# Kernel optimization log

Hardware: AMD Instinct MI355X
Metric: run time of the kernel (lower is better)

Reference implementation:

```python
import jax, jax.numpy as jnp
import numpy as np

N = 50000
E = 800000
D_IN = 64
D_E = 32
H = 128
EPS = 1e-5


def _seg_mean(msgs, dst, n):
    s = jax.ops.segment_sum(msgs, dst, num_segments=n)
    c = jax.ops.segment_sum(jnp.ones((dst.shape[0], 1), msgs.dtype), dst, num_segments=n)
    return s / jnp.maximum(c, 1.0)


def _bn(h, g, b, m, v):
    return g * (h - m) * jax.lax.rsqrt(v + EPS) + b


def setup_inputs() -> dict:
    key = jax.random.key(0)
    ks = jax.random.split(key, 32)
    inp = {
        "x": jax.random.normal(ks[0], (N, D_IN), jnp.float32),
        "edge_index_0": jax.random.randint(ks[1], (2, E), 0, N),
        "edge_index_1": jax.random.randint(ks[2], (2, E), 0, N),
        "edge_index_2": jax.random.randint(ks[3], (2, E), 0, N),
        "edge_attr_0": jax.random.normal(ks[4], (E, D_E), jnp.float32),
        # conv1: Linear(D_IN + D_E -> H)
        "W1": jax.random.normal(ks[5], (H, D_IN + D_E), jnp.float32) * 0.1,
        "b1": jnp.zeros((H,), jnp.float32),
        "g1": jnp.ones((H,), jnp.float32), "be1": jnp.zeros((H,), jnp.float32),
        "m1": jax.random.normal(ks[6], (H,), jnp.float32) * 0.1,
        "v1": jax.random.uniform(ks[7], (H,), jnp.float32) + 0.5,
        # SAGEConv2: lin_l (bias) on aggregated neighbors + lin_r (no bias) on self
        "Wl2": jax.random.normal(ks[8], (H, H), jnp.float32) * 0.1,
        "bl2": jnp.zeros((H,), jnp.float32),
        "Wr2": jax.random.normal(ks[9], (H, H), jnp.float32) * 0.1,
        "g2": jnp.ones((H,), jnp.float32), "be2": jnp.zeros((H,), jnp.float32),
        "m2": jax.random.normal(ks[10], (H,), jnp.float32) * 0.1,
        "v2": jax.random.uniform(ks[11], (H,), jnp.float32) + 0.5,
        # SAGEConv3
        "Wl3": jax.random.normal(ks[12], (H, H), jnp.float32) * 0.1,
        "bl3": jnp.zeros((H,), jnp.float32),
        "Wr3": jax.random.normal(ks[13], (H, H), jnp.float32) * 0.1,
        "g3": jnp.ones((H,), jnp.float32), "be3": jnp.zeros((H,), jnp.float32),
        "m3": jax.random.normal(ks[14], (H,), jnp.float32) * 0.1,
        "v3": jax.random.uniform(ks[15], (H,), jnp.float32) + 0.5,
        # mlp: Linear(H + D_IN -> 64) -> ReLU -> Linear(64 -> 1)
        "W4": jax.random.normal(ks[16], (64, H + D_IN), jnp.float32) * 0.1,
        "b4": jnp.zeros((64,), jnp.float32),
        "W5": jax.random.normal(ks[17], (1, 64), jnp.float32) * 0.1,
        "b5": jnp.zeros((1,), jnp.float32),
    }
    return inp


def reference(x, edge_index_0, edge_index_1, edge_index_2, edge_attr_0,
              W1, b1, g1, be1, m1, v1,
              Wl2, bl2, Wr2, g2, be2, m2, v2,
              Wl3, bl3, Wr3, g3, be3, m3, v3,
              W4, b4, W5, b5):
    n = x.shape[0]
    init = x
    # conv1: gather x_j + edge_attr, concat, linear, mean scatter, relu (update)
    msg = jnp.concatenate([x[edge_index_0[0]], edge_attr_0], axis=-1) @ W1.T + b1  # [E,H]
    h = jax.nn.relu(_seg_mean(msg, edge_index_0[1], n))
    h = jax.nn.relu(_bn(h, g1, be1, m1, v1))  # dropout: eval (identity)
    # conv2: SAGEConv = lin_l(mean_j x_j) + lin_r(x)
    agg = _seg_mean(h[edge_index_1[0]], edge_index_1[1], n)
    h = agg @ Wl2.T + bl2 + h @ Wr2.T
    h = jax.nn.relu(_bn(h, g2, be2, m2, v2))
    # conv3
    agg = _seg_mean(h[edge_index_2[0]], edge_index_2[1], n)
    h = agg @ Wl3.T + bl3 + h @ Wr3.T
    h = jax.nn.relu(_bn(h, g3, be3, m3, v3))
    # readout mlp on [h, initial_embedding]
    z = jnp.concatenate([h, init], axis=1)
    z = jax.nn.relu(z @ W4.T + b4)
    out = (z @ W5.T + b5).squeeze(-1)  # [N]
    return out
```

## Files before the change

kernel.cpp:

```cpp
#include <hip/hip_runtime.h>
#include <hip/hip_bf16.h>
#include <stdint.h>

#define NN 50000
#define NE 800000
#define EPS 1e-5f

#define KB 196
#define SH 8
#define NPB 256
#define RCAP 4500
#define PTP 1024
#define PT2 2048

typedef __attribute__((ext_vector_type(8))) short bf16x8;
typedef __attribute__((ext_vector_type(4))) float floatx4;

static __device__ __forceinline__ float bf2f(unsigned int u){
  union { unsigned int i; float f; } c; c.i = u << 16; return c.f;
}
static __device__ __forceinline__ unsigned short f2bf(float f){
  union { float f; unsigned int i; } c; c.f = f;
  unsigned int x = c.i;
  return (unsigned short)((x + 0x7fffu + ((x >> 16) & 1u)) >> 16);
}

#define CVT_X   3200000
#define CVT_W1  3212288
#define CVT_WL2 3228672
#define CVT_WR2 3245056
#define CVT_WL3 3261440
#define CVT_WR3 3277824
#define CVT_END 3290112
__global__ void k_cvt_all(const float* __restrict__ x,  const float* __restrict__ W1,
                          const float* __restrict__ Wl2, const float* __restrict__ Wr2,
                          const float* __restrict__ Wl3, const float* __restrict__ Wr3,
                          const float* __restrict__ W4,
                          unsigned short* __restrict__ xb,  unsigned short* __restrict__ W1b,
                          unsigned short* __restrict__ Wl2b, unsigned short* __restrict__ Wr2b,
                          unsigned short* __restrict__ Wl3b, unsigned short* __restrict__ Wr3b,
                          unsigned short* __restrict__ W4b, int* __restrict__ gcur){
  int i = blockIdx.x * 256 + threadIdx.x;
  if(i >= CVT_END) return;
  if(i < 3 * KB) gcur[i] = 0;
  if(i < CVT_X)        xb[i] = f2bf(x[i]);
  else if(i < CVT_W1)  W1b[i - CVT_X]    = f2bf(W1[i - CVT_X]);
  else if(i < CVT_WL2) Wl2b[i - CVT_W1]  = f2bf(Wl2[i - CVT_W1]);
  else if(i < CVT_WR2) Wr2b[i - CVT_WL2] = f2bf(Wr2[i - CVT_WL2]);
  else if(i < CVT_WL3) Wl3b[i - CVT_WR2] = f2bf(Wl3[i - CVT_WR2]);
  else if(i < CVT_WR3) Wr3b[i - CVT_WL3] = f2bf(Wr3[i - CVT_WL3]);
  else                 W4b[i - CVT_WR3]  = f2bf(W4[i - CVT_WR3]);
}

__global__ void k_partP(const int* __restrict__ ei, const float* __restrict__ ea,
                        int* __restrict__ gcur,
                        int2* __restrict__ recDS, unsigned int* __restrict__ recEA){
  __shared__ int2 stage[PTP];
  __shared__ int slotAbs[PTP];
  __shared__ int hist[KB], ex[KB], cur[KB], gbase[KB];
  __shared__ int part[256];
  __shared__ int tot;
  int tid = threadIdx.x;
  int tile = blockIdx.x * PTP;
  int cnt_local = NE - tile; if(cnt_local > PTP) cnt_local = PTP;
  for(int i = tid; i < KB; i += 256) hist[i] = 0;
  __syncthreads();
  int dst[4], src[4];
  #pragma unroll
  for(int j = 0; j < 4; j++){
    int t = j * 256 + tid;
    if(t < cnt_local){ src[j] = ei[tile + t]; dst[j] = ei[NE + tile + t]; atomicAdd(&hist[dst[j] >> SH], 1); }
    else dst[j] = -1;
  }
  __syncthreads();
  int c0 = (tid < KB) ? hist[tid] : 0;
  part[tid] = c0;
  __syncthreads();
  for(int d = 1; d < 256; d <<= 1){
    int v = (tid >= d) ? part[tid - d] : 0;
    __syncthreads();
    part[tid] += v;
    __syncthreads();
  }
  if(tid < KB){
    int e = part[tid] - c0;
    ex[tid] = e; cur[tid] = e;
    gbase[tid] = atomicAdd(&gcur[tid], c0);
  }
  if(tid == 255) tot = part[255];
  __syncthreads();
  #pragma unroll
  for(int j = 0; j < 4; j++){
    int t = j * 256 + tid;
    if(dst[j] >= 0){
      int b = dst[j] >> SH;
      int s = atomicAdd(&cur[b], 1);
      stage[s] = make_int2(dst[j], src[j]);
      slotAbs[t] = b * RCAP + gbase[b] + (s - ex[b]);
    }
  }
  __syncthreads();
  for(int s = tid; s < tot; s += 256){
    int2 r = stage[s];
    int b = r.x >> SH;
    recDS[b * RCAP + gbase[b] + (s - ex[b])] = r;
  }
  {
    int g = tid >> 4, li = tid & 15;
    for(int t = g; t < cnt_local; t += 16){
      int ds = slotAbs[t];
      float2 v = *(const float2*)(ea + (size_t)(tile + t) * 32 + li * 2);
      recEA[(size_t)ds * 16 + li] = (unsigned int)f2bf(v.x) | ((unsigned int)f2bf(v.y) << 16);
    }
  }
}

__global__ void k_part(const int* __restrict__ ei, int* __restrict__ gcur, int2* __restrict__ rec){
  __shared__ int2 stage[PT2];
  __shared__ int hist[KB], ex[KB], cur[KB], gbase[KB];
  __shared__ int part[256];
  __shared__ int tot;
  int tid = threadIdx.x;
  int tile = blockIdx.x * PT2;
  for(int i = tid; i < KB; i += 256) hist[i] = 0;
  __syncthreads();
  int dst[8], src[8];
  #pragma unroll
  for(int j = 0; j < 8; j++){
    int e = tile + j * 256 + tid;
    if(e < NE){ src[j] = ei[e]; dst[j] = ei[NE + e]; atomicAdd(&hist[dst[j] >> SH], 1); }
    else dst[j] = -1;
  }
  __syncthreads();
  int c0 = (tid < KB) ? hist[tid] : 0;
  part[tid] = c0;
  __syncthreads();
  for(int d = 1; d < 256; d <<= 1){
    int v = (tid >= d) ? part[tid - d] : 0;
    __syncthreads();
    part[tid] += v;
    __syncthreads();
  }
  if(tid < KB){
    int e = part[tid] - c0;
    ex[tid] = e; cur[tid] = e;
    gbase[tid] = atomicAdd(&gcur[tid], c0);
  }
  if(tid == 255) tot = part[255];
  __syncthreads();
  #pragma unroll
  for(int j = 0; j < 8; j++){
    if(dst[j] >= 0){
      int b = dst[j] >> SH;
      int s = atomicAdd(&cur[b], 1);
      stage[s] = make_int2(dst[j], src[j]);
    }
  }
  __syncthreads();
  for(int s = tid; s < tot; s += 256){
    int2 r = stage[s];
    int b = r.x >> SH;
    rec[b * RCAP + gbase[b] + (s - ex[b])] = r;
  }
}

__global__ void k_build0(const int2* __restrict__ rec, const int* __restrict__ gcnt,
                         int2* __restrict__ adj2, int* __restrict__ rowbeg, int* __restrict__ deg){
  __shared__ int cnt[NPB], cur2[NPB];
  __shared__ int part[256];
  int b = blockIdx.x, tid = threadIdx.x;
  int n0 = b << SH;
  int nr = gcnt[b];
  const int2* r = rec + b * RCAP;
  cnt[tid] = 0;
  __syncthreads();
  for(int k = tid; k < nr; k += 256) atomicAdd(&cnt[r[k].x - n0], 1);
  __syncthreads();
  int c0 = cnt[tid];
  part[tid] = c0;
  __syncthreads();
  for(int d = 1; d < 256; d <<= 1){
    int v = (tid >= d) ? part[tid - d] : 0;
    __syncthreads();
    part[tid] += v;
    __syncthreads();
  }
  int base = part[tid] - c0;
  cur2[tid] = base;
  __syncthreads();
  int n = n0 + tid;
  if(n < NN){ rowbeg[n] = b * RCAP + base; deg[n] = c0; }
  for(int k = tid; k < nr; k += 256){
    int2 q = r[k];
    int p = atomicAdd(&cur2[q.x - n0], 1);
    adj2[b * RCAP + p] = make_int2(q.y, b * RCAP + k);
  }
}

__global__ void k_build(const int2* __restrict__ rec, const int* __restrict__ gcnt,
                        int* __restrict__ adj, int* __restrict__ rowbeg, int* __restrict__ deg){
  __shared__ int cnt[NPB], cur2[NPB];
  __shared__ int part[256];
  int b = blockIdx.x, tid = threadIdx.x;
  int n0 = b << SH;
  int nr = gcnt[b];
  const int2* r = rec + b * RCAP;
  cnt[tid] = 0;
  __syncthreads();
  for(int k = tid; k < nr; k += 256) atomicAdd(&cnt[r[k].x - n0], 1);
  __syncthreads();
  int c0 = cnt[tid];
  part[tid] = c0;
  __syncthreads();
  for(int d = 1; d < 256; d <<= 1){
    int v = (tid >= d) ? part[tid - d] : 0;
    __syncthreads();
    part[tid] += v;
    __syncthreads();
  }
  int base = part[tid] - c0;
  cur2[tid] = base;
  __syncthreads();
  int n = n0 + tid;
  if(n < NN){ rowbeg[n] = b * RCAP + base; deg[n] = c0; }
  for(int k = tid; k < nr; k += 256){
    int2 q = r[k];
    int p = atomicAdd(&cur2[q.x - n0], 1);
    adj[b * RCAP + p] = q.y;
  }
}

__global__ void k_aggXE(const int* __restrict__ rowbeg, const int* __restrict__ deg,
                        const int2* __restrict__ adj2,
                        const unsigned short* __restrict__ xb, const unsigned int* __restrict__ recEA,
                        unsigned short* __restrict__ agg){
  int w = (blockIdx.x * blockDim.x + threadIdx.x) >> 6;
  int lane = threadIdx.x & 63;
  if(w >= NN) return;
  int sub = lane >> 4, li = lane & 15;
  int r0 = rowbeg[w], dg = deg[w], r1 = r0 + dg;
  float acc[8] = {0.f,0.f,0.f,0.f,0.f,0.f,0.f,0.f};
  for(int k = r0; k < r1; k += 8){
    int e0 = k + sub, e1 = k + 4 + sub;
    int i0 = e0 < r1 ? e0 : r1 - 1;
    int i1 = e1 < r1 ? e1 : r1 - 1;
    float m0 = e0 < r1 ? 1.f : 0.f;
    float m1 = e1 < r1 ? 1.f : 0.f;
    int2 a0 = adj2[i0], a1 = adj2[i1];
    if(li < 8){
      uint4 v0 = *(const uint4*)(xb + (size_t)a0.x * 64 + li * 8);
      uint4 v1 = *(const uint4*)(xb + (size_t)a1.x * 64 + li * 8);
      acc[0] += m0 * bf2f(v0.x & 0xffffu); acc[1] += m0 * bf2f(v0.x >> 16);
      acc[2] += m0 * bf2f(v0.y & 0xffffu); acc[3] += m0 * bf2f(v0.y >> 16);
      acc[4] += m0 * bf2f(v0.z & 0xffffu); acc[5] += m0 * bf2f(v0.z >> 16);
      acc[6] += m0 * bf2f(v0.w & 0xffffu); acc[7] += m0 * bf2f(v0.w >> 16);
      acc[0] += m1 * bf2f(v1.x & 0xffffu); acc[1] += m1 * bf2f(v1.x >> 16);
      acc[2] += m1 * bf2f(v1.y & 0xffffu); acc[3] += m1 * bf2f(v1.y >> 16);
      acc[4] += m1 * bf2f(v1.z & 0xffffu); acc[5] += m1 * bf2f(v1.z >> 16);
      acc[6] += m1 * bf2f(v1.w & 0xffffu); acc[7] += m1 * bf2f(v1.w >> 16);
    } else {
      int j = li - 8;
      uint2 p0 = *(const uint2*)(recEA + (size_t)a0.y * 16 + j * 2);
      uint2 p1 = *(const uint2*)(recEA + (size_t)a1.y * 16 + j * 2);
      acc[0] += m0 * bf2f(p0.x & 0xffffu); acc[1] += m0 * bf2f(p0.x >> 16);
      acc[2] += m0 * bf2f(p0.y & 0xffffu); acc[3] += m0 * bf2f(p0.y >> 16);
      acc[0] += m1 * bf2f(p1.x & 0xffffu); acc[1] += m1 * bf2f(p1.x >> 16);
      acc[2] += m1 * bf2f(p1.y & 0xffffu); acc[3] += m1 * bf2f(p1.y >> 16);
    }
  }
  #pragma unroll
  for(int d = 16; d < 64; d <<= 1){
    #pragma unroll
    for(int i = 0; i < 8; i++) acc[i] += __shfl_xor(acc[i], d, 64);
  }
  if(sub == 0){
    float inv = 1.0f / (float)(dg > 0 ? dg : 1);
    if(li < 8){
      unsigned int q0 = (unsigned int)f2bf(acc[0]*inv) | ((unsigned int)f2bf(acc[1]*inv) << 16);
      unsigned int q1 = (unsigned int)f2bf(acc[2]*inv) | ((unsigned int)f2bf(acc[3]*inv) << 16);
      unsigned int q2 = (unsigned int)f2bf(acc[4]*inv) | ((unsigned int)f2bf(acc[5]*inv) << 16);
      unsigned int q3 = (unsigned int)f2bf(acc[6]*inv) | ((unsigned int)f2bf(acc[7]*inv) << 16);
      *(uint4*)(agg + (size_t)w * 96 + li * 8) = make_uint4(q0, q1, q2, q3);
    } else {
      int j = li - 8;
      unsigned int q0 = (unsigned int)f2bf(acc[0]*inv) | ((unsigned int)f2bf(acc[1]*inv) << 16);
      unsigned int q1 = (unsigned int)f2bf(acc[2]*inv) | ((unsigned int)f2bf(acc[3]*inv) << 16);
      *(uint2*)(agg + (size_t)w * 96 + 64 + j * 4) = make_uint2(q0, q1);
    }
  }
}

__global__ void k_aggH(const int* __restrict__ rowbeg, const int* __restrict__ deg,
                       const int* __restrict__ adj,
                       const unsigned short* __restrict__ h, unsigned short* __restrict__ agg){
  int w = (blockIdx.x * blockDim.x + threadIdx.x) >> 6;
  int lane = threadIdx.x & 63;
  if(w >= NN) return;
  int sub = lane >> 4, li = lane & 15;
  int r0 = rowbeg[w], dg = deg[w], r1 = r0 + dg;
  float acc[8] = {0.f,0.f,0.f,0.f,0.f,0.f,0.f,0.f};
  for(int k = r0; k < r1; k += 8){
    int e0 = k + sub, e1 = k + 4 + sub;
    int i0 = e0 < r1 ? e0 : r1 - 1;
    int i1 = e1 < r1 ? e1 : r1 - 1;
    float m0 = e0 < r1 ? 1.f : 0.f;
    float m1 = e1 < r1 ? 1.f : 0.f;
    int s0 = adj[i0], s1 = adj[i1];
    uint4 v0 = *(const uint4*)(h + (size_t)s0 * 128 + li * 8);
    uint4 v1 = *(const uint4*)(h + (size_t)s1 * 128 + li * 8);
    acc[0] += m0 * bf2f(v0.x & 0xffffu); acc[1] += m0 * bf2f(v0.x >> 16);
    acc[2] += m0 * bf2f(v0.y & 0xffffu); acc[3] += m0 * bf2f(v0.y >> 16);
    acc[4] += m0 * bf2f(v0.z & 0xffffu); acc[5] += m0 * bf2f(v0.z >> 16);
    acc[6] += m0 * bf2f(v0.w & 0xffffu); acc[7] += m0 * bf2f(v0.w >> 16);
    acc[0] += m1 * bf2f(v1.x & 0xffffu); acc[1] += m1 * bf2f(v1.x >> 16);
    acc[2] += m1 * bf2f(v1.y & 0xffffu); acc[3] += m1 * bf2f(v1.y >> 16);
    acc[4] += m1 * bf2f(v1.z & 0xffffu); acc[5] += m1 * bf2f(v1.z >> 16);
    acc[6] += m1 * bf2f(v1.w & 0xffffu); acc[7] += m1 * bf2f(v1.w >> 16);
  }
  #pragma unroll
  for(int d = 16; d < 64; d <<= 1){
    #pragma unroll
    for(int i = 0; i < 8; i++) acc[i] += __shfl_xor(acc[i], d, 64);
  }
  if(sub == 0){
    float inv = 1.0f / (float)(dg > 0 ? dg : 1);
    unsigned int p0 = (unsigned int)f2bf(acc[0]*inv) | ((unsigned int)f2bf(acc[1]*inv) << 16);
    unsigned int p1 = (unsigned int)f2bf(acc[2]*inv) | ((unsigned int)f2bf(acc[3]*inv) << 16);
    unsigned int p2 = (unsigned int)f2bf(acc[4]*inv) | ((unsigned int)f2bf(acc[5]*inv) << 16);
    unsigned int p3 = (unsigned int)f2bf(acc[6]*inv) | ((unsigned int)f2bf(acc[7]*inv) << 16);
    *(uint4*)(agg + (size_t)w * 128 + li * 8) = make_uint4(p0, p1, p2, p3);
  }
}

__global__ void k_lin1(const unsigned short* __restrict__ agg, const unsigned short* __restrict__ W1,
                       const float* __restrict__ b1,
                       const float* __restrict__ g1, const float* __restrict__ be1,
                       const float* __restrict__ m1, const float* __restrict__ v1,
                       const int* __restrict__ deg, unsigned short* __restrict__ h1){
  int wave = (blockIdx.x * blockDim.x + threadIdx.x) >> 6;
  int lane = threadIdx.x & 63;
  int mt = wave >> 3, nt = wave & 7;
  if(mt >= 3125) return;
  int node0 = mt * 16;
  int col = lane & 15, quad = lane >> 4;
  int o = nt * 16 + col;
  int arow = node0 + col;
  floatx4 acc = {0.f, 0.f, 0.f, 0.f};
  #pragma unroll
  for(int kc = 0; kc < 3; kc++){
    bf16x8 a = *(const bf16x8*)(agg + arow * 96 + kc * 32 + quad * 8);
    bf16x8 b = *(const bf16x8*)(W1 + o * 96 + kc * 32 + quad * 8);
    acc = __builtin_amdgcn_mfma_f32_16x16x32_bf16(a, b, acc, 0, 0, 0);
  }
  float bb = b1[o];
  float sc = g1[o] * rsqrtf(v1[o] + EPS);
  float mv = m1[o], bev = be1[o];
  #pragma unroll
  for(int r = 0; r < 4; r++){
    int node = node0 + quad * 4 + r;
    float pre = (deg[node] > 0) ? (acc[r] + bb) : 0.0f;
    float t = fmaxf(pre, 0.f);
    float bn = sc * (t - mv) + bev;
    h1[node * 128 + o] = f2bf(fmaxf(bn, 0.f));
  }
}

__global__ void k_sage(const unsigned short* __restrict__ agg, const unsigned short* __restrict__ hin,
                       const unsigned short* __restrict__ Wl, const float* __restrict__ bl,
                       const unsigned short* __restrict__ Wr,
                       const float* __restrict__ g, const float* __restrict__ be,
                       const float* __restrict__ m, const float* __restrict__ v,
                       unsigned short* __restrict__ hout){
  int wave = (blockIdx.x * blockDim.x + threadIdx.x) >> 6;
  int lane = threadIdx.x & 63;
  int mt = wave >> 3, nt = wave & 7;
  if(mt >= 3125) return;
  int node0 = mt * 16;
  int col = lane & 15, quad = lane >> 4;
  int o = nt * 16 + col;
  int arow = node0 + col;
  floatx4 acc = {0.f, 0.f, 0.f, 0.f};
  #pragma unroll
  for(int kc = 0; kc < 4; kc++){
    bf16x8 a = *(const bf16x8*)(agg + arow * 128 + kc * 32 + quad * 8);
    bf16x8 b = *(const bf16x8*)(Wl + o * 128 + kc * 32 + quad * 8);
    acc = __builtin_amdgcn_mfma_f32_16x16x32_bf16(a, b, acc, 0, 0, 0);
  }
  #pragma unroll
  for(int kc = 0; kc < 4; kc++){
    bf16x8 a = *(const bf16x8*)(hin + arow * 128 + kc * 32 + quad * 8);
    bf16x8 b = *(const bf16x8*)(Wr + o * 128 + kc * 32 + quad * 8);
    acc = __builtin_amdgcn_mfma_f32_16x16x32_bf16(a, b, acc, 0, 0, 0);
  }
  float blv = bl[o];
  float sc = g[o] * rsqrtf(v[o] + EPS);
  float mv = m[o], bev = be[o];
  #pragma unroll
  for(int r = 0; r < 4; r++){
    int node = node0 + quad * 4 + r;
    float pre = acc[r] + blv;
    float bn = sc * (pre - mv) + bev;
    hout[node * 128 + o] = f2bf(fmaxf(bn, 0.f));
  }
}

__global__ void k_readout(const unsigned short* __restrict__ h3, const unsigned short* __restrict__ xb,
                          const unsigned short* __restrict__ W4, const float* __restrict__ b4,
                          const float* __restrict__ W5, const float* __restrict__ b5,
                          float* __restrict__ out){
  int wave = (blockIdx.x * blockDim.x + threadIdx.x) >> 6;
  int lane = threadIdx.x & 63;
  if(wave >= 3125) return;
  int node0 = wave * 16;
  int col = lane & 15, quad = lane >> 4;
  int arow = node0 + col;
  float partial[4] = {0.f, 0.f, 0.f, 0.f};
  #pragma unroll
  for(int nt = 0; nt < 4; nt++){
    int o = nt * 16 + col;
    floatx4 acc = {0.f, 0.f, 0.f, 0.f};
    #pragma unroll
    for(int kc = 0; kc < 4; kc++){
      bf16x8 a = *(const bf16x8*)(h3 + arow * 128 + kc * 32 + quad * 8);
      bf16x8 b = *(const bf16x8*)(W4 + o * 192 + kc * 32 + quad * 8);
      acc = __builtin_amdgcn_mfma_f32_16x16x32_bf16(a, b, acc, 0, 0, 0);
    }
    #pragma unroll
    for(int kc = 0; kc < 2; kc++){
      bf16x8 a = *(const bf16x8*)(xb + arow * 64 + kc * 32 + quad * 8);
      bf16x8 b = *(const bf16x8*)(W4 + o * 192 + 128 + kc * 32 + quad * 8);
      acc = __builtin_amdgcn_mfma_f32_16x16x32_bf16(a, b, acc, 0, 0, 0);
    }
    float bb = b4[o];
    float w5 = W5[o];
    #pragma unroll
    for(int r = 0; r < 4; r++)
      partial[r] += fmaxf(acc[r] + bb, 0.f) * w5;
  }
  #pragma unroll
  for(int d = 1; d < 16; d <<= 1){
    #pragma unroll
    for(int r = 0; r < 4; r++)
      partial[r] += __shfl_xor(partial[r], d, 64);
  }
  if(col == 0){
    float b5f = b5[0];
    #pragma unroll
    for(int r = 0; r < 4; r++)
      out[node0 + quad * 4 + r] = partial[r] + b5f;
  }
}

extern "C" void kernel_launch(void* const* d_in, const int* in_sizes, int n_in,
                              void* d_out, int out_size, void* d_ws, size_t ws_size,
                              hipStream_t stream) {
  const float* x   = (const float*)d_in[0];
  const int* ei0   = (const int*)d_in[1];
  const int* ei1   = (const int*)d_in[2];
  const int* ei2   = (const int*)d_in[3];
  const float* ea  = (const float*)d_in[4];
  const float* W1  = (const float*)d_in[5];
  const float* b1  = (const float*)d_in[6];
  const float* g1  = (const float*)d_in[7];
  const float* be1 = (const float*)d_in[8];
  const float* m1  = (const float*)d_in[9];
  const float* v1  = (const float*)d_in[10];
  const float* Wl2 = (const float*)d_in[11];
  const float* bl2 = (const float*)d_in[12];
  const float* Wr2 = (const float*)d_in[13];
  const float* g2  = (const float*)d_in[14];
  const float* be2 = (const float*)d_in[15];
  const float* m2  = (const float*)d_in[16];
  const float* v2  = (const float*)d_in[17];
  const float* Wl3 = (const float*)d_in[18];
  const float* bl3 = (const float*)d_in[19];
  const float* Wr3 = (const float*)d_in[20];
  const float* g3  = (const float*)d_in[21];
  const float* be3 = (const float*)d_in[22];
  const float* m3  = (const float*)d_in[23];
  const float* v3  = (const float*)d_in[24];
  const float* W4  = (const float*)d_in[25];
  const float* b4  = (const float*)d_in[26];
  const float* W5  = (const float*)d_in[27];
  const float* b5  = (const float*)d_in[28];

  char* ws = (char*)d_ws;
  size_t off = 0;
  auto alloc = [&](size_t bytes) -> void* {
    void* p = (void*)(ws + off);
    off += (bytes + 255) & ~(size_t)255;
    return p;
  };
  int* gcur    = (int*)alloc(3 * KB * sizeof(int));
  int* rowbeg3 = (int*)alloc(3 * NN * sizeof(int));
  int* deg3    = (int*)alloc(3 * NN * sizeof(int));
  int2* recDS  = (int2*)alloc((size_t)KB * RCAP * 8);
  int2* adj2   = (int2*)alloc((size_t)KB * RCAP * 8);
  unsigned int* recEA = (unsigned int*)alloc((size_t)KB * RCAP * 64);
  unsigned short* agg1 = (unsigned short*)alloc((size_t)NN * 96 * 2);
  unsigned short* xb   = (unsigned short*)alloc((size_t)NN * 64 * 2);
  unsigned short* W1b  = (unsigned short*)alloc(12288 * 2);
  unsigned short* Wl2b = (unsigned short*)alloc(16384 * 2);
  unsigned short* Wr2b = (unsigned short*)alloc(16384 * 2);
  unsigned short* Wl3b = (unsigned short*)alloc(16384 * 2);
  unsigned short* Wr3b = (unsigned short*)alloc(16384 * 2);
  unsigned short* W4b  = (unsigned short*)alloc(12288 * 2);

  int* adjI = (int*)adj2;

  unsigned short* h1   = (unsigned short*)recEA;
  unsigned short* aggH = h1 + (size_t)NN * 128;
  unsigned short* h2   = h1 + (size_t)2 * NN * 128;
  unsigned short* h3   = h1 + (size_t)3 * NN * 128;

  int* rb0 = rowbeg3;            int* dg0 = deg3;
  int* rb1 = rowbeg3 + NN;       int* dg1 = deg3 + NN;
  int* rb2 = rowbeg3 + 2 * NN;   int* dg2 = deg3 + 2 * NN;

  const int gPP   = (NE + PTP - 1) / PTP;
  const int gP2   = (NE + PT2 - 1) / PT2;
  const int gAgg  = (NN * 64) / 256;
  const int gTile = (3125 * 8 * 64) / 256;
  const int gRead = (3125 * 64 + 255) / 256;
  const int gCvt  = (CVT_END + 255) / 256;

  k_cvt_all<<<gCvt, 256, 0, stream>>>(x, W1, Wl2, Wr2, Wl3, Wr3, W4,
                                      xb, W1b, Wl2b, Wr2b, Wl3b, Wr3b, W4b, gcur);

  k_partP<<<gPP, 256, 0, stream>>>(ei0, ea, gcur, recDS, recEA);
  k_build0<<<KB, 256, 0, stream>>>(recDS, gcur, adj2, rb0, dg0);
  k_aggXE<<<gAgg, 256, 0, stream>>>(rb0, dg0, adj2, xb, recEA, agg1);
  k_lin1<<<gTile, 256, 0, stream>>>(agg1, W1b, b1, g1, be1, m1, v1, dg0, h1);

  k_part<<<gP2, 256, 0, stream>>>(ei1, gcur + KB, recDS);
  k_build<<<KB, 256, 0, stream>>>(recDS, gcur + KB, adjI, rb1, dg1);
  k_aggH<<<gAgg, 256, 0, stream>>>(rb1, dg1, adjI, h1, aggH);
  k_sage<<<gTile, 256, 0, stream>>>(aggH, h1, Wl2b, bl2, Wr2b, g2, be2, m2, v2, h2);

  k_part<<<gP2, 256, 0, stream>>>(ei2, gcur + 2 * KB, recDS);
  k_build<<<KB, 256, 0, stream>>>(recDS, gcur + 2 * KB, adjI, rb2, dg2);
  k_aggH<<<gAgg, 256, 0, stream>>>(rb2, dg2, adjI, h2, aggH);
  k_sage<<<gTile, 256, 0, stream>>>(aggH, h2, Wl3b, bl3, Wr3b, g3, be3, m3, v3, h3);

  k_readout<<<gRead, 256, 0, stream>>>(h3, xb, W4b, b4, W5, b5, (float*)d_out);

  (void)in_sizes; (void)n_in; (void)out_size; (void)ws_size;
}
```

Before: 567.8 us.

## Gather edge attributes directly by original edge id instead of permuting them

The first partition kernel no longer copies and converts the edge-attribute matrix into a bucket-permuted bf16 buffer. It now records each edge's original index, which build0 stores in the adjacency list. The aggregation kernel then gathers fp32 edge attributes straight from the input. This removes a full read-convert-write pass over the edge attributes, but the aggregation now does random fp32 gathers, which are twice the bytes of bf16, and the partition tile grows to 2048 edges.

```diff
diff --git a/kernel.cpp b/kernel.cpp
--- a/kernel.cpp
+++ b/kernel.cpp
@@ -10,7 +10,6 @@
 #define SH 8
 #define NPB 256
 #define RCAP 4500
-#define PTP 1024
 #define PT2 2048
 
 typedef __attribute__((ext_vector_type(8))) short bf16x8;
@@ -52,24 +51,22 @@
   else                 W4b[i - CVT_WR3]  = f2bf(W4[i - CVT_WR3]);
 }
 
-__global__ void k_partP(const int* __restrict__ ei, const float* __restrict__ ea,
-                        int* __restrict__ gcur,
-                        int2* __restrict__ recDS, unsigned int* __restrict__ recEA){
-  __shared__ int2 stage[PTP];
-  __shared__ int slotAbs[PTP];
+__global__ void k_part0(const int* __restrict__ ei, int* __restrict__ gcur,
+                        int2* __restrict__ rec, int* __restrict__ recE){
+  __shared__ int2 stage[PT2];
+  __shared__ int stE[PT2];
   __shared__ int hist[KB], ex[KB], cur[KB], gbase[KB];
   __shared__ int part[256];
   __shared__ int tot;
   int tid = threadIdx.x;
-  int tile = blockIdx.x * PTP;
-  int cnt_local = NE - tile; if(cnt_local > PTP) cnt_local = PTP;
+  int tile = blockIdx.x * PT2;
   for(int i = tid; i < KB; i += 256) hist[i] = 0;
   __syncthreads();
-  int dst[4], src[4];
-  #pragma unroll
-  for(int j = 0; j < 4; j++){
-    int t = j * 256 + tid;
-    if(t < cnt_local){ src[j] = ei[tile + t]; dst[j] = ei[NE + tile + t]; atomicAdd(&hist[dst[j] >> SH], 1); }
+  int dst[8], src[8];
+  #pragma unroll
+  for(int j = 0; j < 8; j++){
+    int e = tile + j * 256 + tid;
+    if(e < NE){ src[j] = ei[e]; dst[j] = ei[NE + e]; atomicAdd(&hist[dst[j] >> SH], 1); }
     else dst[j] = -1;
   }
   __syncthreads();
@@ -90,28 +87,21 @@
   if(tid == 255) tot = part[255];
   __syncthreads();
   #pragma unroll
-  for(int j = 0; j < 4; j++){
-    int t = j * 256 + tid;
+  for(int j = 0; j < 8; j++){
     if(dst[j] >= 0){
       int b = dst[j] >> SH;
       int s = atomicAdd(&cur[b], 1);
       stage[s] = make_int2(dst[j], src[j]);
-      slotAbs[t] = b * RCAP + gbase[b] + (s - ex[b]);
+      stE[s] = tile + j * 256 + tid;
     }
   }
   __syncthreads();
   for(int s = tid; s < tot; s += 256){
     int2 r = stage[s];
     int b = r.x >> SH;
-    recDS[b * RCAP + gbase[b] + (s - ex[b])] = r;
-  }
-  {
-    int g = tid >> 4, li = tid & 15;
-    for(int t = g; t < cnt_local; t += 16){
-      int ds = slotAbs[t];
-      float2 v = *(const float2*)(ea + (size_t)(tile + t) * 32 + li * 2);
-      recEA[(size_t)ds * 16 + li] = (unsigned int)f2bf(v.x) | ((unsigned int)f2bf(v.y) << 16);
-    }
+    int idx = b * RCAP + gbase[b] + (s - ex[b]);
+    rec[idx] = r;
+    recE[idx] = stE[s];
   }
 }
 
@@ -164,7 +154,8 @@
   }
 }
 
-__global__ void k_build0(const int2* __restrict__ rec, const int* __restrict__ gcnt,
+__global__ void k_build0(const int2* __restrict__ rec, const int* __restrict__ recE,
+                         const int* __restrict__ gcnt,
                          int2* __restrict__ adj2, int* __restrict__ rowbeg, int* __restrict__ deg){
   __shared__ int cnt[NPB], cur2[NPB];
   __shared__ int part[256];
@@ -172,6 +163,7 @@
   int n0 = b << SH;
   int nr = gcnt[b];
   const int2* r = rec + b * RCAP;
+  const int* re = recE + b * RCAP;
   cnt[tid] = 0;
   __syncthreads();
   for(int k = tid; k < nr; k += 256) atomicAdd(&cnt[r[k].x - n0], 1);
@@ -193,7 +185,7 @@
   for(int k = tid; k < nr; k += 256){
     int2 q = r[k];
     int p = atomicAdd(&cur2[q.x - n0], 1);
-    adj2[b * RCAP + p] = make_int2(q.y, b * RCAP + k);
+    adj2[b * RCAP + p] = make_int2(q.y, re[k]);
   }
 }
 
@@ -232,7 +224,7 @@
 
 __global__ void k_aggXE(const int* __restrict__ rowbeg, const int* __restrict__ deg,
                         const int2* __restrict__ adj2,
-                        const unsigned short* __restrict__ xb, const unsigned int* __restrict__ recEA,
+                        const unsigned short* __restrict__ xb, const float* __restrict__ ea,
                         unsigned short* __restrict__ agg){
   int w = (blockIdx.x * blockDim.x + threadIdx.x) >> 6;
   int lane = threadIdx.x & 63;
@@ -260,12 +252,12 @@
       acc[6] += m1 * bf2f(v1.w & 0xffffu); acc[7] += m1 * bf2f(v1.w >> 16);
     } else {
       int j = li - 8;
-      uint2 p0 = *(const uint2*)(recEA + (size_t)a0.y * 16 + j * 2);
-      uint2 p1 = *(const uint2*)(recEA + (size_t)a1.y * 16 + j * 2);
-      acc[0] += m0 * bf2f(p0.x & 0xffffu); acc[1] += m0 * bf2f(p0.x >> 16);
-      acc[2] += m0 * bf2f(p0.y & 0xffffu); acc[3] += m0 * bf2f(p0.y >> 16);
-      acc[0] += m1 * bf2f(p1.x & 0xffffu); acc[1] += m1 * bf2f(p1.x >> 16);
-      acc[2] += m1 * bf2f(p1.y & 0xffffu); acc[3] += m1 * bf2f(p1.y >> 16);
+      float4 p0 = *(const float4*)(ea + (size_t)a0.y * 32 + j * 4);
+      float4 p1 = *(const float4*)(ea + (size_t)a1.y * 32 + j * 4);
+      acc[0] += m0 * p0.x; acc[1] += m0 * p0.y;
+      acc[2] += m0 * p0.z; acc[3] += m0 * p0.w;
+      acc[0] += m1 * p1.x; acc[1] += m1 * p1.y;
+      acc[2] += m1 * p1.z; acc[3] += m1 * p1.w;
     }
   }
   #pragma unroll
@@ -496,7 +488,7 @@
   int* deg3    = (int*)alloc(3 * NN * sizeof(int));
   int2* recDS  = (int2*)alloc((size_t)KB * RCAP * 8);
   int2* adj2   = (int2*)alloc((size_t)KB * RCAP * 8);
-  unsigned int* recEA = (unsigned int*)alloc((size_t)KB * RCAP * 64);
+  unsigned short* hbuf = (unsigned short*)alloc((size_t)KB * RCAP * 64);
   unsigned short* agg1 = (unsigned short*)alloc((size_t)NN * 96 * 2);
   unsigned short* xb   = (unsigned short*)alloc((size_t)NN * 64 * 2);
   unsigned short* W1b  = (unsigned short*)alloc(12288 * 2);
@@ -508,16 +500,16 @@
 
   int* adjI = (int*)adj2;
 
-  unsigned short* h1   = (unsigned short*)recEA;
+  unsigned short* h1   = hbuf;
   unsigned short* aggH = h1 + (size_t)NN * 128;
   unsigned short* h2   = h1 + (size_t)2 * NN * 128;
   unsigned short* h3   = h1 + (size_t)3 * NN * 128;
+  int* recE = (int*)((char*)hbuf + (size_t)4 * NN * 128 * 2);
 
   int* rb0 = rowbeg3;            int* dg0 = deg3;
   int* rb1 = rowbeg3 + NN;       int* dg1 = deg3 + NN;
   int* rb2 = rowbeg3 + 2 * NN;   int* dg2 = deg3 + 2 * NN;
 
-  const int gPP   = (NE + PTP - 1) / PTP;
   const int gP2   = (NE + PT2 - 1) / PT2;
   const int gAgg  = (NN * 64) / 256;
   const int gTile = (3125 * 8 * 64) / 256;
@@ -527,9 +519,9 @@
   k_cvt_all<<<gCvt, 256, 0, stream>>>(x, W1, Wl2, Wr2, Wl3, Wr3, W4,
                                       xb, W1b, Wl2b, Wr2b, Wl3b, Wr3b, W4b, gcur);
 
-  k_partP<<<gPP, 256, 0, stream>>>(ei0, ea, gcur, recDS, recEA);
-  k_build0<<<KB, 256, 0, stream>>>(recDS, gcur, adj2, rb0, dg0);
-  k_aggXE<<<gAgg, 256, 0, stream>>>(rb0, dg0, adj2, xb, recEA, agg1);
+  k_part0<<<gP2, 256, 0, stream>>>(ei0, gcur, recDS, recE);
+  k_build0<<<KB, 256, 0, stream>>>(recDS, recE, gcur, adj2, rb0, dg0);
+  k_aggXE<<<gAgg, 256, 0, stream>>>(rb0, dg0, adj2, xb, ea, agg1);
   k_lin1<<<gTile, 256, 0, stream>>>(agg1, W1b, b1, g1, be1, m1, v1, dg0, h1);
 
   k_part<<<gP2, 256, 0, stream>>>(ei1, gcur + KB, recDS);
```

Result: faster. 533.7 us (-6.0%).
